# Kernel tuning notes

Measured on AMD Instinct MI355X. Metric: run time of the kernel, lower is better.

## Reference

```python
import jax, jax.numpy as jnp
import numpy as np
from jax.scipy.special import logsumexp

G, H, L, N, K = 2000, 128, 10, 4096, 10
TAU, LC, LA, EPS = 0.1, 1.0, 0.5, 1e-6

def _lin_init(k, fi, fo):
    return jax.random.normal(k, (fi, fo), jnp.float32) / np.sqrt(fi)

def setup_inputs():
    key = jax.random.key(0)
    ks = jax.random.split(key, 12)
    return {
        'wt_x': jax.random.normal(ks[0], (N, G), jnp.float32),
        'ko_x': jax.random.normal(ks[1], (N, G), jnp.float32),
        'wt_labels': jax.random.randint(ks[2], (N,), 0, K, dtype=jnp.int32),
        'ko_labels': jax.random.randint(ks[3], (N,), 0, K, dtype=jnp.int32),
        'enc_w1': _lin_init(ks[4], G, H), 'enc_b1': jnp.zeros((H,)),
        'enc_g': jnp.ones((H,)), 'enc_be': jnp.zeros((H,)),
        'enc_w2': _lin_init(ks[5], H, L), 'enc_b2': jnp.zeros((L,)),
        'kap_w1': _lin_init(ks[6], G, H), 'kap_b1': jnp.zeros((H,)),
        'kap_g': jnp.ones((H,)), 'kap_be': jnp.zeros((H,)),
        'kap_w2': _lin_init(ks[7], H, 1), 'kap_b2': jnp.zeros((1,)),
        'dec_w1': _lin_init(ks[8], L, H), 'dec_b1': jnp.zeros((H,)),
        'dec_g': jnp.ones((H,)), 'dec_be': jnp.zeros((H,)),
        'dec_w2': _lin_init(ks[9], H, G), 'dec_b2': jnp.zeros((G,)),
    }

def _mlp(x, w1, b1, g, be, w2, b2):
    # Linear -> LayerNorm -> ReLU -> Linear (dropout_prob=0)
    h = x @ w1 + b1
    m = h.mean(-1, keepdims=True)
    v = ((h - m) ** 2).mean(-1, keepdims=True)
    h = (h - m) / jnp.sqrt(v + 1e-5) * g + be
    return jax.nn.relu(h) @ w2 + b2

def _contrastive(z_wt, z_ko, y_wt, y_ko):
    S = (z_wt @ z_ko.T) / TAU  # [Nwt, Nko], unit-norm z so |S| <= 1/tau
    total = jnp.float32(0.0)
    n_shared = jnp.float32(0.0)
    for c in range(K):  # fixed small class count
        mwt = (y_wt == c).astype(S.dtype)
        mko = (y_ko == c).astype(S.dtype)
        n_wt, n_ko = mwt.sum(), mko.sum()
        valid = (n_wt > 0) & (n_ko > 0)
        nw, nk = jnp.maximum(n_wt, 1.0), jnp.maximum(n_ko, 1.0)
        # mean_{i in c, j in c} (LSE_i - S_ij) over ko columns of class c
        lse_r = logsumexp(jnp.where(mko[None, :] > 0, S, -1e4), axis=1)
        l1 = jnp.sum(mwt * (lse_r - (S @ mko) / nk)) / nw
        lse_c = logsumexp(jnp.where(mwt[:, None] > 0, S, -1e4), axis=0)
        l2 = jnp.sum(mko * (lse_c - (mwt @ S) / nw)) / nk
        total = total + jnp.where(valid, 0.5 * (l1 + l2), 0.0)
        n_shared = n_shared + valid.astype(S.dtype)
    return jnp.where(n_shared > 0, total / jnp.maximum(n_shared, 1.0), 0.0)

def _alignment(z, y):
    ones = jnp.ones(z.shape[0], z.dtype)
    counts = jax.ops.segment_sum(ones, y, num_segments=K)
    mu_c = jax.ops.segment_sum(z, y, num_segments=K) / jnp.maximum(counts, 1.0)[:, None]
    dev = z - mu_c[y]
    per_class = jax.ops.segment_sum(jnp.sum(dev ** 2, axis=1), y, num_segments=K) / jnp.maximum(counts, 1.0)
    present = counts > 0
    return jnp.sum(jnp.where(present, per_class, 0.0)) / jnp.maximum(jnp.sum(present.astype(z.dtype)), 1.0)

def reference(wt_x, ko_x, enc_w1, enc_b1, enc_g, enc_be, enc_w2, enc_b2, kap_w1, kap_b1, kap_g, kap_be, kap_w2, kap_b2, dec_w1, dec_b1, dec_g, dec_be, dec_w2, dec_b2, wt_labels, ko_labels):
    def encode(x):
        mu = _mlp(x, enc_w1, enc_b1, enc_g, enc_be, enc_w2, enc_b2)
        mu = mu / jnp.maximum(jnp.linalg.norm(mu, axis=1, keepdims=True), 1e-12)
        kappa = jax.nn.softplus(_mlp(x, kap_w1, kap_b1, kap_g, kap_be, kap_w2, kap_b2)) + EPS
        return mu, kappa
    wt_mu, wt_kappa = encode(wt_x)
    ko_mu, ko_kappa = encode(ko_x)
    wt_z, ko_z = wt_mu, ko_mu  # eval mode: z = mu (deterministic)
    wt_rec = _mlp(wt_z, dec_w1, dec_b1, dec_g, dec_be, dec_w2, dec_b2)
    ko_rec = _mlp(ko_z, dec_w1, dec_b1, dec_g, dec_be, dec_w2, dec_b2)
    recon = jnp.mean((wt_rec - wt_x) ** 2) + jnp.mean((ko_rec - ko_x) ** 2)
    kl = (wt_kappa.mean() + ko_kappa.mean()) * 0.01
    contrast = _contrastive(wt_z, ko_z, wt_labels, ko_labels)
    align = _alignment(jnp.concatenate([wt_z, ko_z], 0), jnp.concatenate([wt_labels, ko_labels], 0))
    return recon + kl + LC * contrast + LA * align
```

## Files before the change

kernel.cpp:

```cpp
#include <hip/hip_runtime.h>
#include <math.h>

typedef __attribute__((ext_vector_type(8))) __bf16 bf16x8;
typedef __attribute__((ext_vector_type(4))) float f32x4;

#define GL2LDS_(gptr, lptr) \
    __builtin_amdgcn_global_load_lds((const __attribute__((address_space(1))) void*)(gptr), \
                                     (__attribute__((address_space(3))) void*)(lptr), 16, 0, 0)

#define OFF_NWT   0
#define OFF_NKO   10
#define OFF_L1    20
#define OFF_L2    30
#define OFF_CNT   40
#define OFF_ZSUM  50
#define OFF_ZSQ   150
#define OFF_KSUM  160
#define OFF_REC   162
#define IOFF_WTOFF 192
#define IOFF_KOOFF 204
#define IOFF_WTCTR 216
#define IOFF_KOCTR 226
#define ACC_FLOATS 256

#define WT_OFF    256
#define WTLO_OFF  (WT_OFF + 262144)
#define H_OFF     (WTLO_OFF + 262144)
#define Z_OFF     (H_OFF + 8192*256)
#define KAP_OFF   (Z_OFF + 8192*10)
#define HREST_OFF (KAP_OFF + 8192)
#define HPART     2097152

#define ACT_HI_OFF  H_OFF
#define ACT_LO_OFF  (H_OFF + 524288)
#define BT_HI_OFF   (H_OFF + 1048576)
#define BT_LO_OFF   (H_OFF + 1179648)
#define ZCKO_OFF    (H_OFF + 1310720)
#define ZCWT_OFF    (H_OFF + 1351680)
#define PART_OFF    (H_OFF + 1392640)

__global__ __launch_bounds__(256) void pack_w_kernel(const float* __restrict__ enc_w1,
                                                     const float* __restrict__ kap_w1,
                                                     __bf16* __restrict__ WThi,
                                                     __bf16* __restrict__ WTlo)
{
    __shared__ float tile[64][65];
    int kt = blockIdx.x & 31;
    int ct = blockIdx.x >> 5;
    int k0 = kt * 64, c0 = ct * 64;
    int t = threadIdx.x;
    int lr = t >> 6, lc = t & 63;
#pragma unroll
    for (int i = 0; i < 16; ++i) {
        int k = k0 + lr + 4 * i;
        int c = c0 + lc;
        float v = 0.f;
        if (k < 2000) v = (c < 128) ? enc_w1[(size_t)k * 128 + c]
                                    : kap_w1[(size_t)k * 128 + (c - 128)];
        tile[lc][lr + 4 * i] = v;
    }
    __syncthreads();
#pragma unroll
    for (int i = 0; i < 16; ++i) {
        int c = c0 + lr + 4 * i;
        int k = k0 + lc;
        float v = tile[lr + 4 * i][lc];
        __bf16 h = (__bf16)v;
        __bf16 l = (__bf16)(v - (float)h);
        size_t idx = (size_t)c * 2048 + k;
        WThi[idx] = h;
        WTlo[idx] = l;
    }
}

__global__ __launch_bounds__(256) void pack_dw2_kernel(const float* __restrict__ dw2,
                                                       __bf16* __restrict__ BThi,
                                                       __bf16* __restrict__ BTlo)
{
    __shared__ float tile[64][129];
    int j0 = blockIdx.x * 64;
    int t = threadIdx.x;
#pragma unroll
    for (int i = 0; i < 32; ++i) {
        int idx = i * 256 + t;
        int c = idx >> 6, jj = idx & 63;
        int j = j0 + jj;
        tile[jj][c] = (j < 2000) ? dw2[(size_t)c * 2000 + j] : 0.f;
    }
    __syncthreads();
#pragma unroll
    for (int i = 0; i < 32; ++i) {
        int idx = i * 256 + t;
        int jj = idx >> 7, c = idx & 127;
        float v = tile[jj][c];
        __bf16 h = (__bf16)v;
        size_t o = (size_t)(j0 + jj) * 128 + c;
        BThi[o] = h;
        BTlo[o] = (__bf16)(v - (float)h);
    }
}

__global__ void counts_kernel(const int* __restrict__ wtl, const int* __restrict__ kol,
                              float* __restrict__ acc)
{
    __shared__ int cw[10], ck[10];
    int t = threadIdx.x;
    if (t < 10) { cw[t] = 0; ck[t] = 0; }
    __syncthreads();
    for (int i = t; i < 4096; i += 1024) {
        atomicAdd(&cw[wtl[i]], 1);
        atomicAdd(&ck[kol[i]], 1);
    }
    __syncthreads();
    if (t < 10) { acc[OFF_NWT + t] = (float)cw[t]; acc[OFF_NKO + t] = (float)ck[t]; }
    if (t == 0) {
        int* ai = (int*)acc;
        int aw = 0, ak = 0;
        for (int c = 0; c < 10; ++c) {
            ai[IOFF_WTOFF + c] = aw; aw += cw[c];
            ai[IOFF_KOOFF + c] = ak; ak += ck[c];
        }
        ai[IOFF_WTOFF + 10] = aw;
        ai[IOFF_KOOFF + 10] = ak;
    }
}

__global__ __launch_bounds__(256) void scatter_z_kernel(const float* __restrict__ Z,
                                                        const int* __restrict__ wtl,
                                                        const int* __restrict__ kol,
                                                        float* __restrict__ acc,
                                                        float* __restrict__ ZcWT,
                                                        float* __restrict__ ZcKO)
{
    __shared__ int lcnt[20];
    __shared__ int lbase[20];
    int t = threadIdx.x;
    if (t < 20) lcnt[t] = 0;
    __syncthreads();
    int row = blockIdx.x * 256 + t;
    int side = row >= 4096;
    int r = side ? row - 4096 : row;
    int c = side ? kol[r] : wtl[r];
    int key = side * 10 + c;
    int myrank = atomicAdd(&lcnt[key], 1);
    __syncthreads();
    int* ai = (int*)acc;
    if (t < 20 && lcnt[t] > 0)
        lbase[t] = atomicAdd(&ai[IOFF_WTCTR + t], lcnt[t]);
    __syncthreads();
    int off = side ? ai[IOFF_KOOFF + c] : ai[IOFF_WTOFF + c];
    int slot = off + lbase[key] + myrank;
    float* dst = side ? ZcKO : ZcWT;
    const float* zr = Z + (size_t)row * 10;
#pragma unroll
    for (int d = 0; d < 10; ++d) dst[d * 4096 + slot] = zr[d];
}

__global__ __launch_bounds__(512) void gemm1_kernel(const float* __restrict__ wt_x,
                                                    const float* __restrict__ ko_x,
                                                    const __bf16* __restrict__ WThi,
                                                    const __bf16* __restrict__ WTlo,
                                                    float* __restrict__ Hb,
                                                    float* __restrict__ Hrest,
                                                    int nkc)
{
    __shared__ short Bs[2][2][2][4096];
    int t = threadIdx.x;
    int widx = t >> 6, lane = t & 63;
    int wm = widx >> 1, wn = widx & 1;
    int b = blockIdx.x;
    int mt = b & 63, strip = (b >> 6) & 1, kc = b >> 7;
    int R0 = mt * 128;
    int cb = strip * 128;
    int kchunk = 2048 / nkc;
    int kbase = kc * kchunk;
    int kleft = 2000 - kbase;
    int nsteps = (kleft < kchunk) ? ((kleft + 31) >> 5) : (kchunk >> 5);
    int ntiles = (nsteps + 1) >> 1;

    const float* xb = (R0 < 4096) ? (wt_x + (size_t)R0 * 2000)
                                  : (ko_x + (size_t)(R0 - 4096) * 2000);
    int ar = wm * 32 + (lane & 15);
    const float* xrow0 = xb + (size_t)ar * 2000 + kbase;
    const float* xrow1 = xrow0 + (size_t)16 * 2000;
    int kboff = (lane >> 4) * 8;

    int col0 = t >> 2;
    int s0   = (t & 3) ^ ((col0 >> 1) & 3);
    size_t boff = (size_t)(cb + col0) * 2048 + kbase + s0 * 8;
    const __bf16* bsrcH = WThi + boff;
    const __bf16* bsrcL = WTlo + boff;

#define STAGEB_(buf, tl) do { \
    int st_ = (tl) * 2; \
    GL2LDS_(bsrcH + (size_t)st_ * 32,       &Bs[buf][0][0][t * 8]); \
    GL2LDS_(bsrcH + (size_t)(st_ + 1) * 32, &Bs[buf][0][1][t * 8]); \
    GL2LDS_(bsrcL + (size_t)st_ * 32,       &Bs[buf][1][0][t * 8]); \
    GL2LDS_(bsrcL + (size_t)(st_ + 1) * 32, &Bs[buf][1][1][t * 8]); } while (0)

    f32x4 acc00, acc01, acc02, acc03;
    f32x4 acc10, acc11, acc12, acc13;
#pragma unroll
    for (int r = 0; r < 4; ++r) {
        acc00[r]=0.f; acc01[r]=0.f; acc02[r]=0.f; acc03[r]=0.f;
        acc10[r]=0.f; acc11[r]=0.f; acc12[r]=0.f; acc13[r]=0.f;
    }

    float4 aA00, aA01, aA10, aA11, aA20, aA21, aA30, aA31;
    float4 aB00, aB01, aB10, aB11, aB20, aB21, aB30, aB31;

#define GLOADA_(step, a00, a01, a10, a11) do { \
    int k0_ = (step) * 32; \
    int k_ = k0_ + kboff; \
    if (kbase + k0_ <= 1952) { \
        a00 = *(const float4*)(xrow0 + k_); \
        a01 = *(const float4*)(xrow0 + k_ + 4); \
        a10 = *(const float4*)(xrow1 + k_); \
        a11 = *(const float4*)(xrow1 + k_ + 4); \
    } else { \
        float t0_[8], t1_[8]; \
        _Pragma("unroll") \
        for (int j = 0; j < 8; ++j) { \
            int kk = kbase + k_ + j; \
            t0_[j] = (kk < 2000) ? xrow0[k_ + j] : 0.f; \
            t1_[j] = (kk < 2000) ? xrow1[k_ + j] : 0.f; } \
        a00 = make_float4(t0_[0], t0_[1], t0_[2], t0_[3]); \
        a01 = make_float4(t0_[4], t0_[5], t0_[6], t0_[7]); \
        a10 = make_float4(t1_[0], t1_[1], t1_[2], t1_[3]); \
        a11 = make_float4(t1_[4], t1_[5], t1_[6], t1_[7]); } } while (0)

#define CONVA_(a0, a1, ahi, alo) do { \
    float av_[8] = {a0.x, a0.y, a0.z, a0.w, a1.x, a1.y, a1.z, a1.w}; \
    _Pragma("unroll") \
    for (int j = 0; j < 8; ++j) { \
        __bf16 h_ = (__bf16)av_[j]; \
        ahi[j] = h_; \
        alo[j] = (__bf16)(av_[j] - (float)h_); } } while (0)

#define MFMAH_(buf, half, ahi0, alo0, ahi1, alo1) do { \
    _Pragma("unroll") \
    for (int nf = 0; nf < 4; ++nf) { \
        bf16x8 bhf = *(const bf16x8*)&Bs[buf][0][half][(ubase + nf * 64) * 8]; \
        bf16x8 blf = *(const bf16x8*)&Bs[buf][1][half][(ubase + nf * 64) * 8]; \
        f32x4* a0 = (nf == 0) ? &acc00 : (nf == 1) ? &acc01 : (nf == 2) ? &acc02 : &acc03; \
        f32x4* a1 = (nf == 0) ? &acc10 : (nf == 1) ? &acc11 : (nf == 2) ? &acc12 : &acc13; \
        *a0 = __builtin_amdgcn_mfma_f32_16x16x32_bf16(ahi0, bhf, *a0, 0, 0, 0); \
        *a0 = __builtin_amdgcn_mfma_f32_16x16x32_bf16(alo0, bhf, *a0, 0, 0, 0); \
        *a0 = __builtin_amdgcn_mfma_f32_16x16x32_bf16(ahi0, blf, *a0, 0, 0, 0); \
        *a1 = __builtin_amdgcn_mfma_f32_16x16x32_bf16(ahi1, bhf, *a1, 0, 0, 0); \
        *a1 = __builtin_amdgcn_mfma_f32_16x16x32_bf16(alo1, bhf, *a1, 0, 0, 0); \
        *a1 = __builtin_amdgcn_mfma_f32_16x16x32_bf16(ahi1, blf, *a1, 0, 0, 0); } } while (0)

    STAGEB_(0, 0);
    GLOADA_(0, aA00, aA01, aA10, aA11);
    GLOADA_(1, aA20, aA21, aA30, aA31);
    if (1 < ntiles) {
        GLOADA_(2, aB00, aB01, aB10, aB11);
        GLOADA_(3, aB20, aB21, aB30, aB31);
    }
    __syncthreads();

    int cpr = lane & 15;
    int pph = (lane >> 4) ^ ((cpr >> 1) & 3);
    int ubase = (wn * 64 + cpr) * 4 + pph;

    int half_iters = (ntiles + 1) >> 1;
    for (int it = 0; it < half_iters; ++it) {
        int tl = it * 2;
        {
            if (tl + 1 < ntiles) STAGEB_(1, tl + 1);
            bf16x8 h00,l00,h01,l01,h10,l10,h11,l11;
            CONVA_(aA00, aA01, h00, l00); CONVA_(aA10, aA11, h01, l01);
            CONVA_(aA20, aA21, h10, l10); CONVA_(aA30, aA31, h11, l11);
            if (tl + 2 < ntiles) {
                GLOADA_(2*(tl+2),   aA00, aA01, aA10, aA11);
                GLOADA_(2*(tl+2)+1, aA20, aA21, aA30, aA31);
            }
            MFMAH_(0, 0, h00, l00, h01, l01);
            MFMAH_(0, 1, h10, l10, h11, l11);
            __syncthreads();
        }
        if (tl + 1 < ntiles) {
            if (tl + 2 < ntiles) STAGEB_(0, tl + 2);
            bf16x8 h00,l00,h01,l01,h10,l10,h11,l11;
            CONVA_(aB00, aB01, h00, l00); CONVA_(aB10, aB11, h01, l01);
            CONVA_(aB20, aB21, h10, l10); CONVA_(aB30, aB31, h11, l11);
            if (tl + 3 < ntiles) {
                GLOADA_(2*(tl+3),   aB00, aB01, aB10, aB11);
                GLOADA_(2*(tl+3)+1, aB20, aB21, aB30, aB31);
            }
            MFMAH_(1, 0, h00, l00, h01, l01);
            MFMAH_(1, 1, h10, l10, h11, l11);
            __syncthreads();
        }
    }

    float* Hq = (kc == 0) ? Hb : (Hrest + (size_t)(kc - 1) * HPART);
#pragma unroll
    for (int r = 0; r < 4; ++r) {
        int row0 = R0 + wm * 32 + (lane >> 4) * 4 + r;
        size_t base0 = (size_t)row0 * 256 + cb + wn * 64 + (lane & 15);
        Hq[base0]      = acc00[r];
        Hq[base0 + 16] = acc01[r];
        Hq[base0 + 32] = acc02[r];
        Hq[base0 + 48] = acc03[r];
        size_t base1 = base0 + (size_t)16 * 256;
        Hq[base1]      = acc10[r];
        Hq[base1 + 16] = acc11[r];
        Hq[base1 + 32] = acc12[r];
        Hq[base1 + 48] = acc13[r];
    }
#undef STAGEB_
#undef GLOADA_
#undef CONVA_
#undef MFMAH_
}

__global__ __launch_bounds__(128) void stage2_kernel(const float* __restrict__ Hb,
    const float* __restrict__ Hrest, int nkc,
    const float* __restrict__ enc_b1, const float* __restrict__ enc_g, const float* __restrict__ enc_be,
    const float* __restrict__ enc_w2, const float* __restrict__ enc_b2,
    const float* __restrict__ kap_b1, const float* __restrict__ kap_g, const float* __restrict__ kap_be,
    const float* __restrict__ kap_w2, const float* __restrict__ kap_b2,
    float* __restrict__ Z, float* __restrict__ Kap)
{
    __shared__ float sh[128];
    int row  = blockIdx.x;
    int wave = threadIdx.x >> 6;
    int lane = threadIdx.x & 63;
    size_t hoff = (size_t)row * 256 + wave * 128;
    const float* hb  = Hb + hoff;
    const float* b1 = wave ? kap_b1 : enc_b1;
    const float* gg = wave ? kap_g  : enc_g;
    const float* bb = wave ? kap_be : enc_be;

    float h0 = hb[lane]      + b1[lane];
    float h1 = hb[lane + 64] + b1[lane + 64];
    for (int j = 0; j + 1 < nkc; ++j) {
        const float* hr = Hrest + (size_t)j * HPART + hoff;
        h0 += hr[lane];
        h1 += hr[lane + 64];
    }
    float s = h0 + h1;
#pragma unroll
    for (int o = 32; o > 0; o >>= 1) s += __shfl_xor(s, o, 64);
    float m = s * (1.f / 128.f);
    float d0 = h0 - m, d1 = h1 - m;
    float v = d0 * d0 + d1 * d1;
#pragma unroll
    for (int o = 32; o > 0; o >>= 1) v += __shfl_xor(v, o, 64);
    v *= (1.f / 128.f);
    float sc = 1.f / sqrtf(v + 1e-5f);
    float r0 = fmaxf(fmaf(d0 * sc, gg[lane],      bb[lane]),      0.f);
    float r1 = fmaxf(fmaf(d1 * sc, gg[lane + 64], bb[lane + 64]), 0.f);

    if (wave == 0) { sh[lane] = r0; sh[lane + 64] = r1; }
    __syncthreads();

    if (wave == 0) {
        float mu = 0.f;
        if (lane < 10) {
            mu = enc_b2[lane];
            for (int c = 0; c < 128; ++c) mu = fmaf(sh[c], enc_w2[c * 10 + lane], mu);
        }
        float n2 = mu * mu;
#pragma unroll
        for (int o = 8; o > 0; o >>= 1) n2 += __shfl_xor(n2, o, 16);
        float inv = 1.f / fmaxf(sqrtf(n2), 1e-12f);
        if (lane < 10) Z[(size_t)row * 10 + lane] = mu * inv;
    } else {
        float p = r0 * kap_w2[lane] + r1 * kap_w2[lane + 64];
#pragma unroll
        for (int o = 32; o > 0; o >>= 1) p += __shfl_xor(p, o, 64);
        if (lane == 0) {
            float x = p + kap_b2[0];
            float sp = (x > 20.f) ? x : log1pf(expf(x));
            Kap[row] = sp + 1e-6f;
        }
    }
}

__global__ __launch_bounds__(256) void dec_act_kernel(const float* __restrict__ Zb,
    const float* __restrict__ dw1, const float* __restrict__ db1,
    const float* __restrict__ dg,  const float* __restrict__ dbe,
    __bf16* __restrict__ Ahi, __bf16* __restrict__ Alo)
{
    int wave = threadIdx.x >> 6;
    int lane = threadIdx.x & 63;
    int row = blockIdx.x * 4 + wave;
    const float* zr = Zb + (size_t)row * 10;
    float z[10];
#pragma unroll
    for (int d = 0; d < 10; ++d) z[d] = zr[d];
    int c0 = lane, c1 = lane + 64;
    float h0 = db1[c0], h1 = db1[c1];
#pragma unroll
    for (int d = 0; d < 10; ++d) {
        h0 = fmaf(z[d], dw1[d * 128 + c0], h0);
        h1 = fmaf(z[d], dw1[d * 128 + c1], h1);
    }
    float s = h0 + h1;
#pragma unroll
    for (int o = 32; o > 0; o >>= 1) s += __shfl_xor(s, o, 64);
    float m = s * (1.f / 128.f);
    float d0 = h0 - m, d1 = h1 - m;
    float v = d0 * d0 + d1 * d1;
#pragma unroll
    for (int o = 32; o > 0; o >>= 1) v += __shfl_xor(v, o, 64);
    v *= (1.f / 128.f);
    float sc = 1.f / sqrtf(v + 1e-5f);
    float a0 = fmaxf(fmaf(d0 * sc, dg[c0], dbe[c0]), 0.f);
    float a1 = fmaxf(fmaf(d1 * sc, dg[c1], dbe[c1]), 0.f);
    __bf16 h0b = (__bf16)a0, h1b = (__bf16)a1;
    size_t base = (size_t)row * 128;
    Ahi[base + c0] = h0b;                 Ahi[base + c1] = h1b;
    Alo[base + c0] = (__bf16)(a0 - (float)h0b);
    Alo[base + c1] = (__bf16)(a1 - (float)h1b);
}

__global__ __launch_bounds__(512, 4) void dec_gemm_kernel(
    const __bf16* __restrict__ Ahi, const __bf16* __restrict__ Alo,
    const __bf16* __restrict__ BThi, const __bf16* __restrict__ BTlo,
    const float* __restrict__ wt_x, const float* __restrict__ ko_x,
    const float* __restrict__ db2, float* __restrict__ acc)
{
    __shared__ short BsH[2][8192];
    __shared__ short BsL[2][8192];
    __shared__ float rs[8];
    int t = threadIdx.x;
    int widx = t >> 6, lane = t & 63;
    int wm = widx >> 2, wn = widx & 3;
    int R0 = (blockIdx.x >> 1) * 32;
    int T0 = (blockIdx.x & 1) * 16;
    const float* xbase = (R0 < 4096) ? wt_x : ko_x;
    int xr0 = ((R0 < 4096) ? R0 : R0 - 4096) + wm * 16 + (lane >> 4) * 4;

    size_t abase = (size_t)(R0 + wm * 16 + (lane & 15)) * 128 + (lane >> 4) * 8;
    bf16x8 ah0 = *(const bf16x8*)(Ahi + abase);
    bf16x8 ah1 = *(const bf16x8*)(Ahi + abase + 32);
    bf16x8 ah2 = *(const bf16x8*)(Ahi + abase + 64);
    bf16x8 ah3 = *(const bf16x8*)(Ahi + abase + 96);
    bf16x8 al0 = *(const bf16x8*)(Alo + abase);
    bf16x8 al1 = *(const bf16x8*)(Alo + abase + 32);
    bf16x8 al2 = *(const bf16x8*)(Alo + abase + 64);
    bf16x8 al3 = *(const bf16x8*)(Alo + abase + 96);

    int g0c = t >> 4,         g0s = t & 15;
    int g1c = (t + 512) >> 4, g1s = t & 15;
    int u0 = g0c * 16 + (g0s ^ (g0c & 7));
    int u1 = g1c * 16 + (g1s ^ (g1c & 7));

    int col_local = wn * 16 + (lane & 15);
    int cl7 = col_local & 7;
    int rb = col_local * 16;
    int sb = lane >> 4;

    uint4 hA0, hA1, lA0, lA1, hB0, hB1, lB0, lB1;

#define GLOADB_(tile, h0, h1, l0, l1) do { \
    size_t gb = (size_t)(tile) * 8192; \
    h0 = *(const uint4*)(BThi + gb + (size_t)t * 8); \
    h1 = *(const uint4*)(BThi + gb + (size_t)(t + 512) * 8); \
    l0 = *(const uint4*)(BTlo + gb + (size_t)t * 8); \
    l1 = *(const uint4*)(BTlo + gb + (size_t)(t + 512) * 8); } while (0)

#define DSWRITE_(buf, h0, h1, l0, l1) do { \
    *(uint4*)&BsH[buf][u0 * 8] = h0; \
    *(uint4*)&BsH[buf][u1 * 8] = h1; \
    *(uint4*)&BsL[buf][u0 * 8] = l0; \
    *(uint4*)&BsL[buf][u1 * 8] = l1; } while (0)

#define COMPUTE_(buf, tile) do { \
    int un0 = rb + ((sb +  0) ^ cl7); \
    int un1 = rb + ((sb +  4) ^ cl7); \
    int un2 = rb + ((sb +  8) ^ cl7); \
    int un3 = rb + ((sb + 12) ^ cl7); \
    bf16x8 bh0 = *(const bf16x8*)&BsH[buf][un0 * 8]; \
    bf16x8 bh1 = *(const bf16x8*)&BsH[buf][un1 * 8]; \
    bf16x8 bh2 = *(const bf16x8*)&BsH[buf][un2 * 8]; \
    bf16x8 bh3 = *(const bf16x8*)&BsH[buf][un3 * 8]; \
    bf16x8 bl0 = *(const bf16x8*)&BsL[buf][un0 * 8]; \
    bf16x8 bl1 = *(const bf16x8*)&BsL[buf][un1 * 8]; \
    bf16x8 bl2 = *(const bf16x8*)&BsL[buf][un2 * 8]; \
    bf16x8 bl3 = *(const bf16x8*)&BsL[buf][un3 * 8]; \
    f32x4 a4; \
    _Pragma("unroll") \
    for (int r = 0; r < 4; ++r) a4[r] = 0.f; \
    a4 = __builtin_amdgcn_mfma_f32_16x16x32_bf16(ah0, bh0, a4, 0, 0, 0); \
    a4 = __builtin_amdgcn_mfma_f32_16x16x32_bf16(al0, bh0, a4, 0, 0, 0); \
    a4 = __builtin_amdgcn_mfma_f32_16x16x32_bf16(ah0, bl0, a4, 0, 0, 0); \
    a4 = __builtin_amdgcn_mfma_f32_16x16x32_bf16(ah1, bh1, a4, 0, 0, 0); \
    a4 = __builtin_amdgcn_mfma_f32_16x16x32_bf16(al1, bh1, a4, 0, 0, 0); \
    a4 = __builtin_amdgcn_mfma_f32_16x16x32_bf16(ah1, bl1, a4, 0, 0, 0); \
    a4 = __builtin_amdgcn_mfma_f32_16x16x32_bf16(ah2, bh2, a4, 0, 0, 0); \
    a4 = __builtin_amdgcn_mfma_f32_16x16x32_bf16(al2, bh2, a4, 0, 0, 0); \
    a4 = __builtin_amdgcn_mfma_f32_16x16x32_bf16(ah2, bl2, a4, 0, 0, 0); \
    a4 = __builtin_amdgcn_mfma_f32_16x16x32_bf16(ah3, bh3, a4, 0, 0, 0); \
    a4 = __builtin_amdgcn_mfma_f32_16x16x32_bf16(al3, bh3, a4, 0, 0, 0); \
    a4 = __builtin_amdgcn_mfma_f32_16x16x32_bf16(ah3, bl3, a4, 0, 0, 0); \
    int col = (tile) * 64 + col_local; \
    if (col < 2000) { \
        float bb = db2[col]; \
        _Pragma("unroll") \
        for (int r = 0; r < 4; ++r) { \
            float xv = xbase[(size_t)(xr0 + r) * 2000 + col]; \
            float e = a4[r] + bb - xv; \
            rsum = fmaf(e, e, rsum); \
        } } } while (0)

    float rsum = 0.f;
    GLOADB_(T0 + 0, hA0, hA1, lA0, lA1);
    GLOADB_(T0 + 1, hB0, hB1, lB0, lB1);
    DSWRITE_(0, hA0, hA1, lA0, lA1);
    __syncthreads();

    for (int it = 0; it < 8; ++it) {
        int lt = it * 2;
        {
            if (lt + 2 < 16) GLOADB_(T0 + lt + 2, hA0, hA1, lA0, lA1);
            DSWRITE_(1, hB0, hB1, lB0, lB1);
            COMPUTE_(0, T0 + lt);
            __syncthreads();
        }
        {
            if (lt + 3 < 16) GLOADB_(T0 + lt + 3, hB0, hB1, lB0, lB1);
            if (lt + 2 < 16) DSWRITE_(0, hA0, hA1, lA0, lA1);
            COMPUTE_(1, T0 + lt + 1);
            __syncthreads();
        }
    }

#pragma unroll
    for (int o = 32; o > 0; o >>= 1) rsum += __shfl_xor(rsum, o, 64);
    if (lane == 0) rs[widx] = rsum;
    __syncthreads();
    if (t == 0) {
        float s = 0.f;
#pragma unroll
        for (int w = 0; w < 8; ++w) s += rs[w];
        atomicAdd(&acc[OFF_REC], s);
    }
#undef GLOADB_
#undef DSWRITE_
#undef COMPUTE_
}

#define MAXNB 768
__global__ __launch_bounds__(256) void contrast_kernel(const float* __restrict__ ZcWT,
                                                       const float* __restrict__ ZcKO,
                                                       float* __restrict__ acc)
{
    __shared__ float zb[MAXNB * 12];
    __shared__ float bsum[4];
    int b = blockIdx.x;
    int cs = b / 3, sub = b - cs * 3;
    int c = cs >> 1, side = cs & 1;
    const int* ai = (const int*)acc;
    int aStart = side ? ai[IOFF_KOOFF + c]     : ai[IOFF_WTOFF + c];
    int aEnd   = side ? ai[IOFF_KOOFF + c + 1] : ai[IOFF_WTOFF + c + 1];
    int bStart = side ? ai[IOFF_WTOFF + c]     : ai[IOFF_KOOFF + c];
    int bEnd   = side ? ai[IOFF_WTOFF + c + 1] : ai[IOFF_KOOFF + c + 1];
    int na = aEnd - aStart;
    int nb = bEnd - bStart;
    if (nb > MAXNB) nb = MAXNB;
    const float* ZA = side ? ZcKO : ZcWT;
    const float* ZB = side ? ZcWT : ZcKO;
    int t = threadIdx.x;

    for (int u = t; u < nb; u += 256) {
#pragma unroll
        for (int d = 0; d < 10; ++d) zb[u * 12 + d] = ZB[d * 4096 + bStart + u];
    }
    __syncthreads();

    int chunk = (na + 2) / 3;
    int r0 = sub * chunk;
    int rcnt = na - r0; if (rcnt > chunk) rcnt = chunk;

    float wsum = 0.f;
    bool waveActive = (nb > 0) && ((t & ~63) < rcnt);
    if (waveActive) {
        bool valid = t < rcnt;
        int ar = aStart + (valid ? (r0 + t) : 0);
        float za[10];
#pragma unroll
        for (int d = 0; d < 10; ++d) za[d] = ZA[d * 4096 + ar];
        float se = 0.f, ss = 0.f;
        for (int u = 0; u < nb; ++u) {
            const float* zp = &zb[u * 12];
            float s = 0.f;
#pragma unroll
            for (int d = 0; d < 10; ++d) s = fmaf(za[d], zp[d], s);
            s *= 10.f;
            se += __expf(s - 10.f);
            ss += s;
        }
        if (valid) wsum = (10.f + __logf(se)) - ss / (float)nb;
    }
#pragma unroll
    for (int o = 32; o > 0; o >>= 1) wsum += __shfl_xor(wsum, o, 64);
    if ((t & 63) == 0) bsum[t >> 6] = wsum;
    __syncthreads();
    if (t == 0) {
        float s = bsum[0] + bsum[1] + bsum[2] + bsum[3];
        if (s != 0.f || nb > 0)
            atomicAdd(&acc[(side ? OFF_L2 : OFF_L1) + c], s);
    }
}

__global__ __launch_bounds__(256) void align_kernel(const float* __restrict__ Z,
                                                    const int* __restrict__ wtl,
                                                    const int* __restrict__ kol,
                                                    const float* __restrict__ Kap,
                                                    float* __restrict__ Part)
{
    __shared__ float cL[10], qL[10], sL[100], ks;
    int t = threadIdx.x;
    if (t < 10) { cL[t] = 0.f; qL[t] = 0.f; }
    if (t < 100) sL[t] = 0.f;
    if (t == 0) ks = 0.f;
    __syncthreads();
    int row = blockIdx.x * 256 + t;
    int c = (row < 4096) ? wtl[row] : kol[row - 4096];
    float zz[10]; float q = 0.f;
#pragma unroll
    for (int d = 0; d < 10; ++d) { zz[d] = Z[(size_t)row * 10 + d]; q = fmaf(zz[d], zz[d], q); }
    atomicAdd(&cL[c], 1.f);
    atomicAdd(&qL[c], q);
#pragma unroll
    for (int d = 0; d < 10; ++d) atomicAdd(&sL[c * 10 + d], zz[d]);
    atomicAdd(&ks, Kap[row]);
    __syncthreads();
    float* pb = Part + (size_t)blockIdx.x * 128;
    if (t < 10)  { pb[t] = cL[t]; pb[10 + t] = qL[t]; }
    if (t < 100) pb[20 + t] = sL[t];
    if (t == 0)  pb[120] = ks;
}

__global__ void finalize_kernel(const float* __restrict__ Part,
                                const float* __restrict__ acc,
                                float* __restrict__ out)
{
    __shared__ float red[121];
    int t = threadIdx.x;
    if (t < 120) {
        float s = 0.f;
        for (int b = 0; b < 32; ++b) s += Part[(size_t)b * 128 + t];
        red[t] = s;
    } else if (t == 120) {
        float s = 0.f;
        for (int b = 0; b < 32; ++b) s += Part[(size_t)b * 128 + 120];
        red[120] = s;
    }
    __syncthreads();
    if (t == 0) {
        float total = 0.f, nsh = 0.f;
        for (int c = 0; c < 10; ++c) {
            float nw = acc[OFF_NWT + c], nk = acc[OFF_NKO + c];
            if (nw > 0.5f && nk > 0.5f) {
                float l1 = acc[OFF_L1 + c] / nw;
                float l2 = acc[OFF_L2 + c] / nk;
                total += 0.5f * (l1 + l2);
                nsh += 1.f;
            }
        }
        float contrast = (nsh > 0.f) ? total / nsh : 0.f;
        float ap = 0.f, np_ = 0.f;
        for (int c = 0; c < 10; ++c) {
            float cn = red[c];
            if (cn > 0.5f) {
                float mu2 = 0.f;
                for (int d = 0; d < 10; ++d) {
                    float mm = red[20 + c * 10 + d] / cn;
                    mu2 = fmaf(mm, mm, mu2);
                }
                ap += red[10 + c] / cn - mu2;
                np_ += 1.f;
            }
        }
        float align = (np_ > 0.f) ? ap / np_ : 0.f;
        float kl = 0.01f * red[120] * (1.f / 4096.f);
        float recon = acc[OFF_REC] * (1.f / 8192000.f);
        out[0] = recon + kl + 1.0f * contrast + 0.5f * align;
    }
}

extern "C" void kernel_launch(void* const* d_in, const int* in_sizes, int n_in,
                              void* d_out, int out_size, void* d_ws, size_t ws_size,
                              hipStream_t stream)
{
    const float* wt_x   = (const float*)d_in[0];
    const float* ko_x   = (const float*)d_in[1];
    const int*   wtl    = (const int*)d_in[2];
    const int*   kol    = (const int*)d_in[3];
    const float* enc_w1 = (const float*)d_in[4];
    const float* enc_b1 = (const float*)d_in[5];
    const float* enc_g  = (const float*)d_in[6];
    const float* enc_be = (const float*)d_in[7];
    const float* enc_w2 = (const float*)d_in[8];
    const float* enc_b2 = (const float*)d_in[9];
    const float* kap_w1 = (const float*)d_in[10];
    const float* kap_b1 = (const float*)d_in[11];
    const float* kap_g  = (const float*)d_in[12];
    const float* kap_be = (const float*)d_in[13];
    const float* kap_w2 = (const float*)d_in[14];
    const float* kap_b2 = (const float*)d_in[15];
    const float* dw1    = (const float*)d_in[16];
    const float* db1    = (const float*)d_in[17];
    const float* dg     = (const float*)d_in[18];
    const float* dbe    = (const float*)d_in[19];
    const float* dw2    = (const float*)d_in[20];
    const float* db2    = (const float*)d_in[21];

    float* ws  = (float*)d_ws;
    float* acc = ws;
    __bf16* WThi = (__bf16*)(ws + WT_OFF);
    __bf16* WTlo = (__bf16*)(ws + WTLO_OFF);
    float* Hb    = ws + H_OFF;
    float* Zb    = ws + Z_OFF;
    float* Kap   = ws + KAP_OFF;
    float* Hrest = ws + HREST_OFF;
    __bf16* Ahi  = (__bf16*)(ws + ACT_HI_OFF);
    __bf16* Alo  = (__bf16*)(ws + ACT_LO_OFF);
    __bf16* BThi = (__bf16*)(ws + BT_HI_OFF);
    __bf16* BTlo = (__bf16*)(ws + BT_LO_OFF);
    float* ZcKO = ws + ZCKO_OFF;
    float* ZcWT = ws + ZCWT_OFF;
    float* Part = ws + PART_OFF;

    size_t need4 = (size_t)(HREST_OFF + 3 * HPART) * sizeof(float);
    int nkc = (ws_size >= need4) ? 4 : 2;

    hipMemsetAsync(acc, 0, ACC_FLOATS * sizeof(float), stream);
    pack_w_kernel<<<128, 256, 0, stream>>>(enc_w1, kap_w1, WThi, WTlo);
    counts_kernel<<<1, 1024, 0, stream>>>(wtl, kol, acc);
    gemm1_kernel<<<128 * nkc, 512, 0, stream>>>(wt_x, ko_x, WThi, WTlo, Hb, Hrest, nkc);
    stage2_kernel<<<8192, 128, 0, stream>>>(Hb, Hrest, nkc, enc_b1, enc_g, enc_be, enc_w2, enc_b2,
                                            kap_b1, kap_g, kap_be, kap_w2, kap_b2, Zb, Kap);
    pack_dw2_kernel<<<32, 256, 0, stream>>>(dw2, BThi, BTlo);
    dec_act_kernel<<<2048, 256, 0, stream>>>(Zb, dw1, db1, dg, dbe, Ahi, Alo);
    scatter_z_kernel<<<32, 256, 0, stream>>>(Zb, wtl, kol, acc, ZcWT, ZcKO);
    contrast_kernel<<<60, 256, 0, stream>>>(ZcWT, ZcKO, acc);
    align_kernel<<<32, 256, 0, stream>>>(Zb, wtl, kol, Kap, Part);
    dec_gemm_kernel<<<512, 512, 0, stream>>>(Ahi, Alo, BThi, BTlo, wt_x, ko_x, db2, acc);
    finalize_kernel<<<1, 128, 0, stream>>>(Part, acc, (float*)d_out);
}
```

Baseline: 174.5 us.

## Fuse decoder first layer into stage2 and merge scatter with align kernel

Moves the decoder's first linear layer plus LayerNorm, ReLU and the bf16 hi/lo split into stage2_kernel, so each row's normalized z is consumed from shared memory instead of being reloaded by a separate dec_act launch. The z scatter for the contrastive loss and the alignment partial sums now run in one kernel that reads Z once. Two launches and their redundant reads go away. The activation and scratch buffers move to a tail region past Hrest, which needs a larger workspace before the 4-chunk split is chosen. Stage2 also gains extra barriers per row.

```diff
diff --git a/kernel.cpp b/kernel.cpp
--- a/kernel.cpp
+++ b/kernel.cpp
@@ -12,32 +12,19 @@
 #define OFF_NKO   10
 #define OFF_L1    20
 #define OFF_L2    30
-#define OFF_CNT   40
-#define OFF_ZSUM  50
-#define OFF_ZSQ   150
-#define OFF_KSUM  160
 #define OFF_REC   162
 #define IOFF_WTOFF 192
 #define IOFF_KOOFF 204
 #define IOFF_WTCTR 216
-#define IOFF_KOCTR 226
 #define ACC_FLOATS 256
 
 #define WT_OFF    256
 #define WTLO_OFF  (WT_OFF + 262144)
 #define H_OFF     (WTLO_OFF + 262144)
-#define Z_OFF     (H_OFF + 8192*256)
-#define KAP_OFF   (Z_OFF + 8192*10)
+#define Z_OFF     (H_OFF + 2097152)
+#define KAP_OFF   (Z_OFF + 81920)
 #define HREST_OFF (KAP_OFF + 8192)
 #define HPART     2097152
-
-#define ACT_HI_OFF  H_OFF
-#define ACT_LO_OFF  (H_OFF + 524288)
-#define BT_HI_OFF   (H_OFF + 1048576)
-#define BT_LO_OFF   (H_OFF + 1179648)
-#define ZCKO_OFF    (H_OFF + 1310720)
-#define ZCWT_OFF    (H_OFF + 1351680)
-#define PART_OFF    (H_OFF + 1392640)
 
 __global__ __launch_bounds__(256) void pack_w_kernel(const float* __restrict__ enc_w1,
                                                      const float* __restrict__ kap_w1,
@@ -123,37 +110,6 @@
         ai[IOFF_WTOFF + 10] = aw;
         ai[IOFF_KOOFF + 10] = ak;
     }
-}
-
-__global__ __launch_bounds__(256) void scatter_z_kernel(const float* __restrict__ Z,
-                                                        const int* __restrict__ wtl,
-                                                        const int* __restrict__ kol,
-                                                        float* __restrict__ acc,
-                                                        float* __restrict__ ZcWT,
-                                                        float* __restrict__ ZcKO)
-{
-    __shared__ int lcnt[20];
-    __shared__ int lbase[20];
-    int t = threadIdx.x;
-    if (t < 20) lcnt[t] = 0;
-    __syncthreads();
-    int row = blockIdx.x * 256 + t;
-    int side = row >= 4096;
-    int r = side ? row - 4096 : row;
-    int c = side ? kol[r] : wtl[r];
-    int key = side * 10 + c;
-    int myrank = atomicAdd(&lcnt[key], 1);
-    __syncthreads();
-    int* ai = (int*)acc;
-    if (t < 20 && lcnt[t] > 0)
-        lbase[t] = atomicAdd(&ai[IOFF_WTCTR + t], lcnt[t]);
-    __syncthreads();
-    int off = side ? ai[IOFF_KOOFF + c] : ai[IOFF_WTOFF + c];
-    int slot = off + lbase[key] + myrank;
-    float* dst = side ? ZcKO : ZcWT;
-    const float* zr = Z + (size_t)row * 10;
-#pragma unroll
-    for (int d = 0; d < 10; ++d) dst[d * 4096 + slot] = zr[d];
 }
 
 __global__ __launch_bounds__(512) void gemm1_kernel(const float* __restrict__ wt_x,
@@ -242,14 +198,14 @@
     for (int nf = 0; nf < 4; ++nf) { \
         bf16x8 bhf = *(const bf16x8*)&Bs[buf][0][half][(ubase + nf * 64) * 8]; \
         bf16x8 blf = *(const bf16x8*)&Bs[buf][1][half][(ubase + nf * 64) * 8]; \
-        f32x4* a0 = (nf == 0) ? &acc00 : (nf == 1) ? &acc01 : (nf == 2) ? &acc02 : &acc03; \
-        f32x4* a1 = (nf == 0) ? &acc10 : (nf == 1) ? &acc11 : (nf == 2) ? &acc12 : &acc13; \
-        *a0 = __builtin_amdgcn_mfma_f32_16x16x32_bf16(ahi0, bhf, *a0, 0, 0, 0); \
-        *a0 = __builtin_amdgcn_mfma_f32_16x16x32_bf16(alo0, bhf, *a0, 0, 0, 0); \
-        *a0 = __builtin_amdgcn_mfma_f32_16x16x32_bf16(ahi0, blf, *a0, 0, 0, 0); \
-        *a1 = __builtin_amdgcn_mfma_f32_16x16x32_bf16(ahi1, bhf, *a1, 0, 0, 0); \
-        *a1 = __builtin_amdgcn_mfma_f32_16x16x32_bf16(alo1, bhf, *a1, 0, 0, 0); \
-        *a1 = __builtin_amdgcn_mfma_f32_16x16x32_bf16(ahi1, blf, *a1, 0, 0, 0); } } while (0)
+        f32x4* p0 = (nf == 0) ? &acc00 : (nf == 1) ? &acc01 : (nf == 2) ? &acc02 : &acc03; \
+        f32x4* p1 = (nf == 0) ? &acc10 : (nf == 1) ? &acc11 : (nf == 2) ? &acc12 : &acc13; \
+        *p0 = __builtin_amdgcn_mfma_f32_16x16x32_bf16(ahi0, bhf, *p0, 0, 0, 0); \
+        *p0 = __builtin_amdgcn_mfma_f32_16x16x32_bf16(alo0, bhf, *p0, 0, 0, 0); \
+        *p0 = __builtin_amdgcn_mfma_f32_16x16x32_bf16(ahi0, blf, *p0, 0, 0, 0); \
+        *p1 = __builtin_amdgcn_mfma_f32_16x16x32_bf16(ahi1, bhf, *p1, 0, 0, 0); \
+        *p1 = __builtin_amdgcn_mfma_f32_16x16x32_bf16(alo1, bhf, *p1, 0, 0, 0); \
+        *p1 = __builtin_amdgcn_mfma_f32_16x16x32_bf16(ahi1, blf, *p1, 0, 0, 0); } } while (0)
 
     STAGEB_(0, 0);
     GLOADA_(0, aA00, aA01, aA10, aA11);
@@ -322,9 +278,14 @@
     const float* __restrict__ enc_w2, const float* __restrict__ enc_b2,
     const float* __restrict__ kap_b1, const float* __restrict__ kap_g, const float* __restrict__ kap_be,
     const float* __restrict__ kap_w2, const float* __restrict__ kap_b2,
-    float* __restrict__ Z, float* __restrict__ Kap)
+    const float* __restrict__ dw1, const float* __restrict__ db1,
+    const float* __restrict__ dg,  const float* __restrict__ dbe,
+    float* __restrict__ Z, float* __restrict__ Kap,
+    __bf16* __restrict__ Ahi, __bf16* __restrict__ Alo)
 {
     __shared__ float sh[128];
+    __shared__ float shz[10];
+    __shared__ float dred[2], dvar[2];
     int row  = blockIdx.x;
     int wave = threadIdx.x >> 6;
     int lane = threadIdx.x & 63;
@@ -367,7 +328,11 @@
 #pragma unroll
         for (int o = 8; o > 0; o >>= 1) n2 += __shfl_xor(n2, o, 16);
         float inv = 1.f / fmaxf(sqrtf(n2), 1e-12f);
-        if (lane < 10) Z[(size_t)row * 10 + lane] = mu * inv;
+        if (lane < 10) {
+            float zv = mu * inv;
+            Z[(size_t)row * 10 + lane] = zv;
+            shz[lane] = zv;
+        }
     } else {
         float p = r0 * kap_w2[lane] + r1 * kap_w2[lane + 64];
 #pragma unroll
@@ -378,44 +343,85 @@
             Kap[row] = sp + 1e-6f;
         }
     }
-}
-
-__global__ __launch_bounds__(256) void dec_act_kernel(const float* __restrict__ Zb,
-    const float* __restrict__ dw1, const float* __restrict__ db1,
-    const float* __restrict__ dg,  const float* __restrict__ dbe,
-    __bf16* __restrict__ Ahi, __bf16* __restrict__ Alo)
-{
-    int wave = threadIdx.x >> 6;
-    int lane = threadIdx.x & 63;
-    int row = blockIdx.x * 4 + wave;
-    const float* zr = Zb + (size_t)row * 10;
-    float z[10];
-#pragma unroll
-    for (int d = 0; d < 10; ++d) z[d] = zr[d];
-    int c0 = lane, c1 = lane + 64;
-    float h0 = db1[c0], h1 = db1[c1];
-#pragma unroll
-    for (int d = 0; d < 10; ++d) {
-        h0 = fmaf(z[d], dw1[d * 128 + c0], h0);
-        h1 = fmaf(z[d], dw1[d * 128 + c1], h1);
-    }
-    float s = h0 + h1;
-#pragma unroll
-    for (int o = 32; o > 0; o >>= 1) s += __shfl_xor(s, o, 64);
-    float m = s * (1.f / 128.f);
-    float d0 = h0 - m, d1 = h1 - m;
-    float v = d0 * d0 + d1 * d1;
-#pragma unroll
-    for (int o = 32; o > 0; o >>= 1) v += __shfl_xor(v, o, 64);
-    v *= (1.f / 128.f);
-    float sc = 1.f / sqrtf(v + 1e-5f);
-    float a0 = fmaxf(fmaf(d0 * sc, dg[c0], dbe[c0]), 0.f);
-    float a1 = fmaxf(fmaf(d1 * sc, dg[c1], dbe[c1]), 0.f);
-    __bf16 h0b = (__bf16)a0, h1b = (__bf16)a1;
-    size_t base = (size_t)row * 128;
-    Ahi[base + c0] = h0b;                 Ahi[base + c1] = h1b;
-    Alo[base + c0] = (__bf16)(a0 - (float)h0b);
-    Alo[base + c1] = (__bf16)(a1 - (float)h1b);
+    __syncthreads();
+
+    {
+        float z[10];
+#pragma unroll
+        for (int d = 0; d < 10; ++d) z[d] = shz[d];
+        int c = threadIdx.x;
+        float h = db1[c];
+#pragma unroll
+        for (int d = 0; d < 10; ++d) h = fmaf(z[d], dw1[d * 128 + c], h);
+        float s2 = h;
+#pragma unroll
+        for (int o = 32; o > 0; o >>= 1) s2 += __shfl_xor(s2, o, 64);
+        if (lane == 0) dred[wave] = s2;
+        __syncthreads();
+        float m2 = (dred[0] + dred[1]) * (1.f / 128.f);
+        float dd = h - m2;
+        float v2 = dd * dd;
+#pragma unroll
+        for (int o = 32; o > 0; o >>= 1) v2 += __shfl_xor(v2, o, 64);
+        if (lane == 0) dvar[wave] = v2;
+        __syncthreads();
+        float var = (dvar[0] + dvar[1]) * (1.f / 128.f);
+        float sc2 = 1.f / sqrtf(var + 1e-5f);
+        float a = fmaxf(fmaf(dd * sc2, dg[c], dbe[c]), 0.f);
+        __bf16 hb_ = (__bf16)a;
+        size_t base = (size_t)row * 128 + c;
+        Ahi[base] = hb_;
+        Alo[base] = (__bf16)(a - (float)hb_);
+    }
+}
+
+__global__ __launch_bounds__(256) void scatter_align_kernel(const float* __restrict__ Z,
+                                                            const int* __restrict__ wtl,
+                                                            const int* __restrict__ kol,
+                                                            const float* __restrict__ Kap,
+                                                            float* __restrict__ acc,
+                                                            float* __restrict__ ZcWT,
+                                                            float* __restrict__ ZcKO,
+                                                            float* __restrict__ Part)
+{
+    __shared__ int lcnt[20];
+    __shared__ int lbase[20];
+    __shared__ float cL[10], qL[10], sL[100], ks;
+    int t = threadIdx.x;
+    if (t < 20) lcnt[t] = 0;
+    if (t < 10) { cL[t] = 0.f; qL[t] = 0.f; }
+    if (t >= 20 && t < 120) sL[t - 20] = 0.f;
+    if (t == 120) ks = 0.f;
+    __syncthreads();
+    int row = blockIdx.x * 256 + t;
+    int side = row >= 4096;
+    int r = side ? row - 4096 : row;
+    int c = side ? kol[r] : wtl[r];
+    int key = side * 10 + c;
+    int myrank = atomicAdd(&lcnt[key], 1);
+    float zz[10]; float q = 0.f;
+    const float* zr = Z + (size_t)row * 10;
+#pragma unroll
+    for (int d = 0; d < 10; ++d) { zz[d] = zr[d]; q = fmaf(zz[d], zz[d], q); }
+    atomicAdd(&cL[c], 1.f);
+    atomicAdd(&qL[c], q);
+#pragma unroll
+    for (int d = 0; d < 10; ++d) atomicAdd(&sL[c * 10 + d], zz[d]);
+    atomicAdd(&ks, Kap[row]);
+    __syncthreads();
+    int* ai = (int*)acc;
+    if (t < 20 && lcnt[t] > 0)
+        lbase[t] = atomicAdd(&ai[IOFF_WTCTR + t], lcnt[t]);
+    __syncthreads();
+    int off = side ? ai[IOFF_KOOFF + c] : ai[IOFF_WTOFF + c];
+    int slot = off + lbase[key] + myrank;
+    float* dst = side ? ZcKO : ZcWT;
+#pragma unroll
+    for (int d = 0; d < 10; ++d) dst[d * 4096 + slot] = zz[d];
+    float* pb = Part + (size_t)blockIdx.x * 128;
+    if (t < 10)  { pb[t] = cL[t]; pb[10 + t] = qL[t]; }
+    if (t < 100) pb[20 + t] = sL[t];
+    if (t == 0)  pb[120] = ks;
 }
 
 __global__ __launch_bounds__(512, 4) void dec_gemm_kernel(
@@ -608,35 +614,6 @@
     }
 }
 
-__global__ __launch_bounds__(256) void align_kernel(const float* __restrict__ Z,
-                                                    const int* __restrict__ wtl,
-                                                    const int* __restrict__ kol,
-                                                    const float* __restrict__ Kap,
-                                                    float* __restrict__ Part)
-{
-    __shared__ float cL[10], qL[10], sL[100], ks;
-    int t = threadIdx.x;
-    if (t < 10) { cL[t] = 0.f; qL[t] = 0.f; }
-    if (t < 100) sL[t] = 0.f;
-    if (t == 0) ks = 0.f;
-    __syncthreads();
-    int row = blockIdx.x * 256 + t;
-    int c = (row < 4096) ? wtl[row] : kol[row - 4096];
-    float zz[10]; float q = 0.f;
-#pragma unroll
-    for (int d = 0; d < 10; ++d) { zz[d] = Z[(size_t)row * 10 + d]; q = fmaf(zz[d], zz[d], q); }
-    atomicAdd(&cL[c], 1.f);
-    atomicAdd(&qL[c], q);
-#pragma unroll
-    for (int d = 0; d < 10; ++d) atomicAdd(&sL[c * 10 + d], zz[d]);
-    atomicAdd(&ks, Kap[row]);
-    __syncthreads();
-    float* pb = Part + (size_t)blockIdx.x * 128;
-    if (t < 10)  { pb[t] = cL[t]; pb[10 + t] = qL[t]; }
-    if (t < 100) pb[20 + t] = sL[t];
-    if (t == 0)  pb[120] = ks;
-}
-
 __global__ void finalize_kernel(const float* __restrict__ Part,
                                 const float* __restrict__ acc,
                                 float* __restrict__ out)
@@ -720,28 +697,30 @@
     float* Zb    = ws + Z_OFF;
     float* Kap   = ws + KAP_OFF;
     float* Hrest = ws + HREST_OFF;
-    __bf16* Ahi  = (__bf16*)(ws + ACT_HI_OFF);
-    __bf16* Alo  = (__bf16*)(ws + ACT_LO_OFF);
-    __bf16* BThi = (__bf16*)(ws + BT_HI_OFF);
-    __bf16* BTlo = (__bf16*)(ws + BT_LO_OFF);
-    float* ZcKO = ws + ZCKO_OFF;
-    float* ZcWT = ws + ZCWT_OFF;
-    float* Part = ws + PART_OFF;
-
-    size_t need4 = (size_t)(HREST_OFF + 3 * HPART) * sizeof(float);
+
+    const size_t TAIL = 2 * 524288 + 2 * 131072 + 2 * 40960 + 4096;
+    size_t need4 = (size_t)(HREST_OFF + 3 * HPART + TAIL) * sizeof(float);
     int nkc = (ws_size >= need4) ? 4 : 2;
+
+    float* tail = ws + HREST_OFF + (size_t)(nkc - 1) * HPART;
+    __bf16* Ahi  = (__bf16*)tail;
+    __bf16* Alo  = (__bf16*)(tail + 524288);
+    __bf16* BThi = (__bf16*)(tail + 1048576);
+    __bf16* BTlo = (__bf16*)(tail + 1048576 + 131072);
+    float* ZcKO = tail + 1048576 + 262144;
+    float* ZcWT = ZcKO + 40960;
+    float* Part = ZcWT + 40960;
 
     hipMemsetAsync(acc, 0, ACC_FLOATS * sizeof(float), stream);
     pack_w_kernel<<<128, 256, 0, stream>>>(enc_w1, kap_w1, WThi, WTlo);
     counts_kernel<<<1, 1024, 0, stream>>>(wtl, kol, acc);
     gemm1_kernel<<<128 * nkc, 512, 0, stream>>>(wt_x, ko_x, WThi, WTlo, Hb, Hrest, nkc);
     stage2_kernel<<<8192, 128, 0, stream>>>(Hb, Hrest, nkc, enc_b1, enc_g, enc_be, enc_w2, enc_b2,
-                                            kap_b1, kap_g, kap_be, kap_w2, kap_b2, Zb, Kap);
+                                            kap_b1, kap_g, kap_be, kap_w2, kap_b2,
+                                            dw1, db1, dg, dbe, Zb, Kap, Ahi, Alo);
     pack_dw2_kernel<<<32, 256, 0, stream>>>(dw2, BThi, BTlo);
-    dec_act_kernel<<<2048, 256, 0, stream>>>(Zb, dw1, db1, dg, dbe, Ahi, Alo);
-    scatter_z_kernel<<<32, 256, 0, stream>>>(Zb, wtl, kol, acc, ZcWT, ZcKO);
+    scatter_align_kernel<<<32, 256, 0, stream>>>(Zb, wtl, kol, Kap, acc, ZcWT, ZcKO, Part);
     contrast_kernel<<<60, 256, 0, stream>>>(ZcWT, ZcKO, acc);
-    align_kernel<<<32, 256, 0, stream>>>(Zb, wtl, kol, Kap, Part);
     dec_gemm_kernel<<<512, 512, 0, stream>>>(Ahi, Alo, BThi, BTlo, wt_x, ko_x, db2, acc);
     finalize_kernel<<<1, 128, 0, stream>>>(Part, acc, (float*)d_out);
 }
```

After: 171.4 us, median of 2. About the same (-1.8%).
